# Performance work log

Measured on AMD Instinct MI355X. Metric: run time of the kernel, lower is better.

The kernel has to match this reference:

```python
import jax, jax.numpy as jnp
import numpy as np

N_NODES = 50000
NEG_SLOPE = 0.2

def _gat_conv(x, W, att_src, att_dst, bias, src, dst):
    # x: [N, in_c] -> h: [N, out_c]
    h = x @ W
    a_src = (h * att_src).sum(-1)  # [N]
    a_dst = (h * att_dst).sum(-1)  # [N]
    e = a_src[src] + a_dst[dst]    # [E]
    e = jnp.where(e > 0, e, NEG_SLOPE * e)  # LeakyReLU
    # segment softmax over destination node neighborhoods
    emax = jax.ops.segment_max(e, dst, num_segments=N_NODES)
    ee = jnp.exp(e - emax[dst])
    denom = jax.ops.segment_sum(ee, dst, num_segments=N_NODES)
    alpha = ee / denom[dst]        # [E]
    out = jax.ops.segment_sum(h[src] * alpha[:, None], dst, num_segments=N_NODES)
    return out + bias

def _with_self_loops(edge_index):
    # PyG GATConv default add_self_loops=True
    loop = jnp.arange(N_NODES, dtype=edge_index.dtype)
    src = jnp.concatenate([edge_index[0], loop])
    dst = jnp.concatenate([edge_index[1], loop])
    return src, dst

def setup_inputs() -> dict:
    key = jax.random.key(0)
    ks = jax.random.split(key, 11)
    in_c, hid_c, out_c = 256, 128, 64
    E = 800000
    x = jax.random.normal(ks[0], (N_NODES, in_c), dtype=jnp.float32)
    edge_index = jax.random.randint(ks[1], (2, E), 0, N_NODES, dtype=jnp.int64)
    s1 = 1.0 / np.sqrt(in_c)
    s2 = 1.0 / np.sqrt(hid_c)
    return {
        "x": x,
        "edge_index": edge_index,
        "W1": jax.random.normal(ks[2], (in_c, hid_c), dtype=jnp.float32) * s1,
        "att_src1": jax.random.normal(ks[3], (hid_c,), dtype=jnp.float32) * s2,
        "att_dst1": jax.random.normal(ks[4], (hid_c,), dtype=jnp.float32) * s2,
        "b1": jax.random.normal(ks[5], (hid_c,), dtype=jnp.float32) * 0.01,
        "W2": jax.random.normal(ks[6], (hid_c, out_c), dtype=jnp.float32) * s2,
        "att_src2": jax.random.normal(ks[7], (out_c,), dtype=jnp.float32) * (1.0 / np.sqrt(out_c)),
        "att_dst2": jax.random.normal(ks[8], (out_c,), dtype=jnp.float32) * (1.0 / np.sqrt(out_c)),
        "b2": jax.random.normal(ks[9], (out_c,), dtype=jnp.float32) * 0.01,
    }

def reference(x, edge_index, W1, att_src1, att_dst1, b1, W2, att_src2, att_dst2, b2):
    src, dst = _with_self_loops(edge_index)
    hid = _gat_conv(x, W1, att_src1, att_dst1, b1, src, dst)
    hid = jax.nn.relu(hid)
    out = _gat_conv(hid, W2, att_src2, att_dst2, b2, src, dst)
    return jax.nn.log_softmax(out, axis=1)
```

## Files before the change

### kernel.cpp

```cpp
#include <hip/hip_runtime.h>
#include <hip/hip_bf16.h>
#include <math.h>

#define N_NODES 50000
#define E_RAW   800000
#define E_TOT   850000
#define NEG_SLOPE 0.2f
#define CAP 64

#define NBKT   392
#define BCAP   2944
#define SCHUNK 4096
#define SB     208

typedef __attribute__((ext_vector_type(8))) short short8;
typedef __attribute__((ext_vector_type(4))) float f32x4;
typedef __attribute__((ext_vector_type(4))) unsigned short ushort4_t;

__device__ __forceinline__ short f2bf(float f) {
    __hip_bfloat16 h = __float2bfloat16(f);
    return *reinterpret_cast<short*>(&h);
}
__device__ __forceinline__ unsigned int f2bfu(float f) {
    __hip_bfloat16 h = __float2bfloat16(f);
    return (unsigned int)*reinterpret_cast<unsigned short*>(&h);
}
__device__ __forceinline__ float bflo(unsigned int u) {
    return __uint_as_float(u << 16);
}
__device__ __forceinline__ float bfhi(unsigned int u) {
    return __uint_as_float(u & 0xffff0000u);
}
__device__ __forceinline__ void fma8(float al, const uint4& h, float* acc) {
    acc[0] = fmaf(al, bflo(h.x), acc[0]);
    acc[1] = fmaf(al, bfhi(h.x), acc[1]);
    acc[2] = fmaf(al, bflo(h.y), acc[2]);
    acc[3] = fmaf(al, bfhi(h.y), acc[3]);
    acc[4] = fmaf(al, bflo(h.z), acc[4]);
    acc[5] = fmaf(al, bfhi(h.z), acc[5]);
    acc[6] = fmaf(al, bflo(h.w), acc[6]);
    acc[7] = fmaf(al, bfhi(h.w), acc[7]);
}
__device__ __forceinline__ void fma4(float al, const uint2& h, float* acc) {
    acc[0] = fmaf(al, bflo(h.x), acc[0]);
    acc[1] = fmaf(al, bfhi(h.x), acc[1]);
    acc[2] = fmaf(al, bflo(h.y), acc[2]);
    acc[3] = fmaf(al, bfhi(h.y), acc[3]);
}

template<int K, int N>
__device__ __forceinline__ void wf_body(
        int idx, const float* __restrict__ W, short* __restrict__ Wf) {
    constexpr int NT = N / 16;
    const int j  = idx & 7;
    const int n  = (idx >> 3) & 15;
    const int q  = (idx >> 7) & 3;
    const int t  = (idx >> 9) % NT;
    const int kc = idx / (512 * NT);
    const int k   = kc * 32 + q * 8 + j;
    const int col = t * 16 + n;
    Wf[idx] = f2bf(W[(size_t)k * N + col]);
}

__global__ __launch_bounds__(256) void gat_wf12_kernel(
        const float* __restrict__ W1, short* __restrict__ Wf1,
        const float* __restrict__ W2, short* __restrict__ Wf2,
        int* __restrict__ gcnt) {
    if (blockIdx.x == 0) {
        gcnt[threadIdx.x] = 0;
        gcnt[threadIdx.x + 256] = 0;
    }
    int idx = blockIdx.x * 256 + threadIdx.x;
    if (idx < 256 * 128) {
        wf_body<256, 128>(idx, W1, Wf1);
    } else {
        idx -= 256 * 128;
        if (idx < 128 * 64) wf_body<128, 64>(idx, W2, Wf2);
    }
}

template<int K, int N>
__device__ __forceinline__ void gemm_att_body(
        const int blk,
        const float* __restrict__ xf, const short* __restrict__ Wf,
        const float* __restrict__ att_src, const float* __restrict__ att_dst,
        short* __restrict__ h_bf,
        float* __restrict__ a_src, float* __restrict__ a_dst) {
    constexpr int NT = N / 16;
    constexpr int KC = K / 32;
    constexpr int PF = KC < 4 ? KC : 4;
    const int tid  = threadIdx.x;
    const int lane = tid & 63;
    const int wv   = tid >> 6;
    const int mrow = lane & 15;
    const int q    = lane >> 4;

    const int row0 = blk * 64 + wv * 16;
    const int rowA = row0 + mrow;
    const int rowAc = rowA < N_NODES ? rowA : 0;
    const float* xrow = &xf[(size_t)rowAc * K + q * 8];

    f32x4 acc[NT];
    #pragma unroll
    for (int t = 0; t < NT; ++t) acc[t] = f32x4{0.f, 0.f, 0.f, 0.f};

    float4 xa[PF], xb[PF];
    #pragma unroll
    for (int kc = 0; kc < PF; ++kc) {
        xa[kc] = *(const float4*)&xrow[kc * 32];
        xb[kc] = *(const float4*)&xrow[kc * 32 + 4];
    }

    #pragma unroll
    for (int kc = 0; kc < KC; ++kc) {
        const int sl = kc % PF;
        short8 a;
        a[0] = f2bf(xa[sl].x); a[1] = f2bf(xa[sl].y);
        a[2] = f2bf(xa[sl].z); a[3] = f2bf(xa[sl].w);
        a[4] = f2bf(xb[sl].x); a[5] = f2bf(xb[sl].y);
        a[6] = f2bf(xb[sl].z); a[7] = f2bf(xb[sl].w);
        if (kc + PF < KC) {
            xa[sl] = *(const float4*)&xrow[(kc + PF) * 32];
            xb[sl] = *(const float4*)&xrow[(kc + PF) * 32 + 4];
        }
        #pragma unroll
        for (int t = 0; t < NT; ++t) {
            const short8 b = *(const short8*)&Wf[((size_t)(kc * NT + t) * 64 + lane) * 8];
            acc[t] = __builtin_amdgcn_mfma_f32_16x16x32_bf16(a, b, acc[t], 0, 0, 0);
        }
    }

    #pragma unroll
    for (int r = 0; r < 4; ++r) {
        const int rowD = row0 + q * 4 + r;
        float ps = 0.0f, pd = 0.0f;
        #pragma unroll
        for (int t = 0; t < NT; ++t) {
            const int col = t * 16 + mrow;
            ps = fmaf(acc[t][r], att_src[col], ps);
            pd = fmaf(acc[t][r], att_dst[col], pd);
        }
        #pragma unroll
        for (int off = 8; off > 0; off >>= 1) {
            ps += __shfl_xor(ps, off);
            pd += __shfl_xor(pd, off);
        }
        if (rowD < N_NODES) {
            if (mrow == 0) { a_src[rowD] = ps; a_dst[rowD] = pd; }
            #pragma unroll
            for (int t = 0; t < NT; ++t)
                h_bf[(size_t)rowD * N + t * 16 + mrow] = f2bf(acc[t][r]);
        }
    }
}

template<int K, int N>
__global__ __launch_bounds__(256) void gat_fat1_kernel(
        const float* __restrict__ xf, const short* __restrict__ Wf,
        const float* __restrict__ att_src, const float* __restrict__ att_dst,
        short* __restrict__ h_bf,
        float* __restrict__ a_src, float* __restrict__ a_dst,
        const int* __restrict__ ei, int* __restrict__ gcnt,
        unsigned int* __restrict__ buf, int GB) {
    __shared__ int hist[NBKT];
    __shared__ int base[NBKT];
    if ((int)blockIdx.x < GB) {
        gemm_att_body<K, N>(blockIdx.x, xf, Wf,
                            att_src, att_dst, h_bf, a_src, a_dst);
    } else {
        const int sb = (int)blockIdx.x - GB;
        const int c0 = sb * SCHUNK;
        const int c1 = (c0 + SCHUNK < E_TOT) ? c0 + SCHUNK : E_TOT;
        for (int t = threadIdx.x; t < NBKT; t += 256) hist[t] = 0;
        __syncthreads();
        for (int i = c0 + threadIdx.x; i < c1; i += 256) {
            const int d = (i < E_RAW) ? ei[E_RAW + i] : (i - E_RAW);
            atomicAdd(&hist[d >> 7], 1);
        }
        __syncthreads();
        for (int t = threadIdx.x; t < NBKT; t += 256)
            base[t] = atomicAdd(&gcnt[t], hist[t]);
        __syncthreads();
        for (int t = threadIdx.x; t < NBKT; t += 256) hist[t] = 0;
        __syncthreads();
        for (int i = c0 + threadIdx.x; i < c1; i += 256) {
            int s, d;
            if (i < E_RAW) { s = ei[i]; d = ei[E_RAW + i]; }
            else           { s = d = i - E_RAW; }
            const int b = d >> 7;
            const int p = base[b] + atomicAdd(&hist[b], 1);
            if (p < BCAP)
                buf[(size_t)b * BCAP + p] =
                    ((unsigned int)s << 7) | (unsigned int)(d & 127);
        }
    }
}

__global__ __launch_bounds__(256) void gat_ell_kernel(
        const unsigned int* __restrict__ buf, const int* __restrict__ gcnt,
        int* __restrict__ cnt, unsigned short* __restrict__ srcs) {
    const int b = blockIdx.x;
    __shared__ unsigned int c2[128];
    if (threadIdx.x < 128) c2[threadIdx.x] = 0;
    __syncthreads();
    int n = gcnt[b];
    n = n < BCAP ? n : BCAP;
    const unsigned int* bb = buf + (size_t)b * BCAP;
    for (int i = threadIdx.x; i < n; i += 256) {
        const unsigned int e = bb[i];
        const int dl = (int)(e & 127u);
        const unsigned int s = e >> 7;
        const unsigned int c = atomicAdd(&c2[dl], 1u);
        if (c < CAP)
            srcs[((size_t)((b << 7) + dl) << 6) + c] = (unsigned short)s;
    }
    __syncthreads();
    const int d = (b << 7) + threadIdx.x;
    if (threadIdx.x < 128 && d < N_NODES) {
        unsigned int c = c2[threadIdx.x];
        cnt[d] = (int)(c < CAP ? c : CAP);
    }
}

__device__ __forceinline__ void softmax_stage(
        const int* __restrict__ cnt, const unsigned short* __restrict__ srcs,
        const float* __restrict__ a_src, const float* __restrict__ a_dst,
        const int d0, float* lalpha, unsigned short* lsrc,
        int* ldeg, float* ladst) {
    const int tid = threadIdx.x;
    if (tid < 16) {
        const int d = d0 + tid;
        int dg = cnt[d];
        ldeg[tid]  = dg < CAP ? dg : CAP;
        ladst[tid] = a_dst[d];
    }
    __syncthreads();
    const int dl = tid >> 4;
    const int so = (tid & 15) * 4;
    const int dg = ldeg[dl];
    const float ad = ladst[dl];
    const ushort4_t s4 =
        *(const ushort4_t*)(srcs + ((size_t)(d0 + dl) << 6) + so);
    float e[4];
    #pragma unroll
    for (int i = 0; i < 4; ++i) {
        if (so + i < dg) {
            const float t = a_src[(int)s4[i]] + ad;
            e[i] = t > 0.0f ? t : NEG_SLOPE * t;
        } else {
            e[i] = -1e30f;
        }
    }
    float m = fmaxf(fmaxf(e[0], e[1]), fmaxf(e[2], e[3]));
    #pragma unroll
    for (int off = 1; off < 16; off <<= 1) m = fmaxf(m, __shfl_xor(m, off));
    float ex[4], ss = 0.0f;
    #pragma unroll
    for (int i = 0; i < 4; ++i) { ex[i] = __expf(e[i] - m); ss += ex[i]; }
    #pragma unroll
    for (int off = 1; off < 16; off <<= 1) ss += __shfl_xor(ss, off);
    const float rinv = 1.0f / ss;
    float4 av;
    av.x = ex[0] * rinv; av.y = ex[1] * rinv;
    av.z = ex[2] * rinv; av.w = ex[3] * rinv;
    *(float4*)&lalpha[(dl << 6) + so] = av;
    *(ushort4_t*)&lsrc[(dl << 6) + so] = s4;
}

__global__ __launch_bounds__(256, 8) void gat_aggr1_fused_kernel(
        const int* __restrict__ cnt, const unsigned short* __restrict__ srcs,
        const float* __restrict__ a_src, const float* __restrict__ a_dst,
        const unsigned short* __restrict__ h_bf, const float* __restrict__ bias,
        const short* __restrict__ Wf2,
        const float* __restrict__ att_src2, const float* __restrict__ att_dst2,
        short* __restrict__ hbf2,
        float* __restrict__ a_src2, float* __restrict__ a_dst2) {
    constexpr int N = 128;
    __shared__ __align__(16) float lalpha[1024];
    __shared__ __align__(16) unsigned short lsrc[1024];
    __shared__ int   ldeg[16];
    __shared__ float ladst[16];
    __shared__ __align__(16) short lh[16 * 136];
    __shared__ float pspart[64], pdpart[64];
    const int tid = threadIdx.x;
    const int d0 = blockIdx.x * 16;

    softmax_stage(cnt, srcs, a_src, a_dst, d0, lalpha, lsrc, ldeg, ladst);
    __syncthreads();

    const int lane = tid & 63;
    const int g    = lane >> 4;
    const int sub  = lane & 15;
    const int dl   = (tid >> 6) * 4 + g;
    const int deg  = ldeg[dl];
    const int base = dl << 6;

    float acc[8];
    #pragma unroll
    for (int c = 0; c < 8; ++c) acc[c] = 0.0f;

    int j = 0;
    for (; j + 4 <= deg; j += 4) {
        const ushort4_t s4 = *(const ushort4_t*)&lsrc[base + j];
        const float4    a4 = *(const float4*)&lalpha[base + j];
        const uint4 h0 = *(const uint4*)(h_bf + (size_t)s4[0] * N + sub * 8);
        const uint4 h1 = *(const uint4*)(h_bf + (size_t)s4[1] * N + sub * 8);
        const uint4 h2 = *(const uint4*)(h_bf + (size_t)s4[2] * N + sub * 8);
        const uint4 h3 = *(const uint4*)(h_bf + (size_t)s4[3] * N + sub * 8);
        fma8(a4.x, h0, acc); fma8(a4.y, h1, acc);
        fma8(a4.z, h2, acc); fma8(a4.w, h3, acc);
    }
    if (j < deg) {
        const ushort4_t s4 = *(const ushort4_t*)&lsrc[base + j];
        const float4    a4 = *(const float4*)&lalpha[base + j];
        const int rem = deg - j;
        const uint4 h0 = *(const uint4*)(h_bf + (size_t)s4[0] * N + sub * 8);
        uint4 h1 = {0, 0, 0, 0}, h2 = {0, 0, 0, 0};
        if (rem >= 2) h1 = *(const uint4*)(h_bf + (size_t)s4[1] * N + sub * 8);
        if (rem >= 3) h2 = *(const uint4*)(h_bf + (size_t)s4[2] * N + sub * 8);
        fma8(a4.x, h0, acc); fma8(a4.y, h1, acc); fma8(a4.z, h2, acc);
    }

    {
        const float4 b0 = *(const float4*)&bias[sub * 8];
        const float4 b1 = *(const float4*)&bias[sub * 8 + 4];
        float v[8];
        v[0] = fmaxf(acc[0] + b0.x, 0.0f); v[1] = fmaxf(acc[1] + b0.y, 0.0f);
        v[2] = fmaxf(acc[2] + b0.z, 0.0f); v[3] = fmaxf(acc[3] + b0.w, 0.0f);
        v[4] = fmaxf(acc[4] + b1.x, 0.0f); v[5] = fmaxf(acc[5] + b1.y, 0.0f);
        v[6] = fmaxf(acc[6] + b1.z, 0.0f); v[7] = fmaxf(acc[7] + b1.w, 0.0f);
        uint4 p;
        p.x = f2bfu(v[0]) | (f2bfu(v[1]) << 16);
        p.y = f2bfu(v[2]) | (f2bfu(v[3]) << 16);
        p.z = f2bfu(v[4]) | (f2bfu(v[5]) << 16);
        p.w = f2bfu(v[6]) | (f2bfu(v[7]) << 16);
        *(uint4*)&lh[dl * 136 + sub * 8] = p;
    }
    __syncthreads();

    const int w    = tid >> 6;
    const int q    = lane >> 4;
    const int mrow = lane & 15;
    f32x4 acc2 = f32x4{0.f, 0.f, 0.f, 0.f};
    #pragma unroll
    for (int kc = 0; kc < 4; ++kc) {
        const short8 a = *(const short8*)&lh[mrow * 136 + q * 8 + kc * 32];
        const short8 b = *(const short8*)&Wf2[((size_t)(kc * 4 + w) * 64 + lane) * 8];
        acc2 = __builtin_amdgcn_mfma_f32_16x16x32_bf16(a, b, acc2, 0, 0, 0);
    }

    const float as2 = att_src2[w * 16 + mrow];
    const float ad2 = att_dst2[w * 16 + mrow];
    #pragma unroll
    for (int r = 0; r < 4; ++r) {
        const int rl = q * 4 + r;
        float ps = acc2[r] * as2;
        float pd = acc2[r] * ad2;
        #pragma unroll
        for (int off = 1; off < 16; off <<= 1) {
            ps += __shfl_xor(ps, off);
            pd += __shfl_xor(pd, off);
        }
        if (mrow == 0) { pspart[w * 16 + rl] = ps; pdpart[w * 16 + rl] = pd; }
        hbf2[(size_t)(d0 + rl) * 64 + w * 16 + mrow] = f2bf(acc2[r]);
    }
    __syncthreads();
    if (tid < 16) {
        a_src2[d0 + tid] = pspart[tid] + pspart[16 + tid]
                         + pspart[32 + tid] + pspart[48 + tid];
        a_dst2[d0 + tid] = pdpart[tid] + pdpart[16 + tid]
                         + pdpart[32 + tid] + pdpart[48 + tid];
    }
}

__global__ __launch_bounds__(256, 8) void gat_aggr2_kernel(
        const int* __restrict__ cnt, const unsigned short* __restrict__ srcs,
        const float* __restrict__ a_src, const float* __restrict__ a_dst,
        const unsigned short* __restrict__ h_bf, const float* __restrict__ bias,
        float* __restrict__ outf) {
    constexpr int N = 64;
    __shared__ __align__(16) float lalpha[1024];
    __shared__ __align__(16) unsigned short lsrc[1024];
    __shared__ int   ldeg[16];
    __shared__ float ladst[16];
    const int tid = threadIdx.x;
    const int d0 = blockIdx.x * 16;

    softmax_stage(cnt, srcs, a_src, a_dst, d0, lalpha, lsrc, ldeg, ladst);
    __syncthreads();

    const int lane = tid & 63;
    const int g    = lane >> 4;
    const int sub  = lane & 15;
    const int dl   = (tid >> 6) * 4 + g;
    const int d    = d0 + dl;
    const int deg  = ldeg[dl];
    const int base = dl << 6;

    float acc[4];
    #pragma unroll
    for (int c = 0; c < 4; ++c) acc[c] = 0.0f;

    int j = 0;
    for (; j + 4 <= deg; j += 4) {
        const ushort4_t s4 = *(const ushort4_t*)&lsrc[base + j];
        const float4    a4 = *(const float4*)&lalpha[base + j];
        const uint2 h0 = *(const uint2*)(h_bf + (size_t)s4[0] * N + sub * 4);
        const uint2 h1 = *(const uint2*)(h_bf + (size_t)s4[1] * N + sub * 4);
        const uint2 h2 = *(const uint2*)(h_bf + (size_t)s4[2] * N + sub * 4);
        const uint2 h3 = *(const uint2*)(h_bf + (size_t)s4[3] * N + sub * 4);
        fma4(a4.x, h0, acc); fma4(a4.y, h1, acc);
        fma4(a4.z, h2, acc); fma4(a4.w, h3, acc);
    }
    if (j < deg) {
        const ushort4_t s4 = *(const ushort4_t*)&lsrc[base + j];
        const float4    a4 = *(const float4*)&lalpha[base + j];
        const int rem = deg - j;
        const uint2 h0 = *(const uint2*)(h_bf + (size_t)s4[0] * N + sub * 4);
        uint2 h1 = {0, 0}, h2 = {0, 0};
        if (rem >= 2) h1 = *(const uint2*)(h_bf + (size_t)s4[1] * N + sub * 4);
        if (rem >= 3) h2 = *(const uint2*)(h_bf + (size_t)s4[2] * N + sub * 4);
        fma4(a4.x, h0, acc); fma4(a4.y, h1, acc); fma4(a4.z, h2, acc);
    }

    float v[4];
    #pragma unroll
    for (int c = 0; c < 4; ++c) v[c] = acc[c] + bias[sub * 4 + c];
    float mm = fmaxf(fmaxf(v[0], v[1]), fmaxf(v[2], v[3]));
    #pragma unroll
    for (int off = 1; off < 16; off <<= 1) mm = fmaxf(mm, __shfl_xor(mm, off));
    float es = __expf(v[0] - mm) + __expf(v[1] - mm)
             + __expf(v[2] - mm) + __expf(v[3] - mm);
    #pragma unroll
    for (int off = 1; off < 16; off <<= 1) es += __shfl_xor(es, off);
    const float ls = logf(es);
    float4 o;
    o.x = v[0] - mm - ls; o.y = v[1] - mm - ls;
    o.z = v[2] - mm - ls; o.w = v[3] - mm - ls;
    *(float4*)&outf[(size_t)d * N + sub * 4] = o;
}

extern "C" void kernel_launch(void* const* d_in, const int* in_sizes, int n_in,
                              void* d_out, int out_size, void* d_ws, size_t ws_size,
                              hipStream_t stream) {
    const float* x        = (const float*)d_in[0];
    const int*   ei       = (const int*)  d_in[1];
    const float* W1       = (const float*)d_in[2];
    const float* att_src1 = (const float*)d_in[3];
    const float* att_dst1 = (const float*)d_in[4];
    const float* b1       = (const float*)d_in[5];
    const float* W2       = (const float*)d_in[6];
    const float* att_src2 = (const float*)d_in[7];
    const float* att_dst2 = (const float*)d_in[8];
    const float* b2       = (const float*)d_in[9];
    float* out = (float*)d_out;
    float* ws  = (float*)d_ws;

    float* a_src1 = ws;
    float* a_dst1 = a_src1 + 50000;
    float* a_src2 = a_dst1 + 50000;
    float* a_dst2 = a_src2 + 50000;
    int*   cnt    = (int*)(a_dst2 + 50000);
    int*   gcnt   = cnt + 50000;
    unsigned int*   buf  = (unsigned int*)(gcnt + 512);
    unsigned short* srcs = (unsigned short*)(buf + (size_t)NBKT * BCAP);
    short* hbf1   = (short*)(srcs + (size_t)N_NODES * CAP);
    short* hbf2   = hbf1  + 6400000;
    short* Wf1    = hbf2  + 3200000;
    short* Wf2    = Wf1   + 32768;

    const int GB = (N_NODES + 63) / 64;

    gat_wf12_kernel<<<160, 256, 0, stream>>>(W1, Wf1, W2, Wf2, gcnt);

    gat_fat1_kernel<256, 128><<<GB + SB, 256, 0, stream>>>(
        x, Wf1, att_src1, att_dst1, hbf1, a_src1, a_dst1,
        ei, gcnt, buf, GB);

    gat_ell_kernel<<<NBKT, 256, 0, stream>>>(buf, gcnt, cnt, srcs);

    gat_aggr1_fused_kernel<<<3125, 256, 0, stream>>>(
        cnt, srcs, a_src1, a_dst1, (const unsigned short*)hbf1, b1,
        Wf2, att_src2, att_dst2, hbf2, a_src2, a_dst2);

    gat_aggr2_kernel<<<3125, 256, 0, stream>>>(
        cnt, srcs, a_src2, a_dst2, (const unsigned short*)hbf2, b2,
        out);
}
```

Baseline: 200.7 us.

## Split layer-1 aggregation into column-sliced kernel plus separate layer-2 GEMM

The fused layer-1 aggregation plus layer-2 GEMM kernel is split in two. A column-sliced aggregation kernel launches four times as many blocks, each handling a 32-column slice and splitting edges across lanes with a shuffle reduction, and writes relu(agg+bias) to a new bf16 buffer. A separate MFMA GEMM kernel then produces h2, with a_src2/a_dst2 computed from precomputed W2·att vectors. Padded source indices (set to 0) let both aggregation loops drop their remainder branches. The split adds a 12.8MB round trip through global memory and an extra launch, and the softmax stage is recomputed once per slice.

Result: slower. 221.8 us (+10.5%).

```diff
diff --git a/kernel.cpp b/kernel.cpp
--- a/kernel.cpp
+++ b/kernel.cpp
@@ -30,6 +30,9 @@
 }
 __device__ __forceinline__ float bfhi(unsigned int u) {
     return __uint_as_float(u & 0xffff0000u);
+}
+__device__ __forceinline__ float bf2f(short v) {
+    return __uint_as_float(((unsigned int)(unsigned short)v) << 16);
 }
 __device__ __forceinline__ void fma8(float al, const uint4& h, float* acc) {
     acc[0] = fmaf(al, bflo(h.x), acc[0]);
@@ -65,10 +68,22 @@
 __global__ __launch_bounds__(256) void gat_wf12_kernel(
         const float* __restrict__ W1, short* __restrict__ Wf1,
         const float* __restrict__ W2, short* __restrict__ Wf2,
+        const float* __restrict__ att_src2, const float* __restrict__ att_dst2,
+        float* __restrict__ wtS, float* __restrict__ wtD,
         int* __restrict__ gcnt) {
     if (blockIdx.x == 0) {
         gcnt[threadIdx.x] = 0;
         gcnt[threadIdx.x + 256] = 0;
+        if (threadIdx.x < 128) {
+            float s = 0.0f, d = 0.0f;
+            for (int n = 0; n < 64; ++n) {
+                const float w = W2[threadIdx.x * 64 + n];
+                s = fmaf(w, att_src2[n], s);
+                d = fmaf(w, att_dst2[n], d);
+            }
+            wtS[threadIdx.x] = s;
+            wtD[threadIdx.x] = d;
+        }
     }
     int idx = blockIdx.x * 256 + threadIdx.x;
     if (idx < 256 * 128) {
@@ -242,13 +257,16 @@
     const ushort4_t s4 =
         *(const ushort4_t*)(srcs + ((size_t)(d0 + dl) << 6) + so);
     float e[4];
+    ushort4_t s4w;
     #pragma unroll
     for (int i = 0; i < 4; ++i) {
         if (so + i < dg) {
             const float t = a_src[(int)s4[i]] + ad;
             e[i] = t > 0.0f ? t : NEG_SLOPE * t;
+            s4w[i] = s4[i];
         } else {
             e[i] = -1e30f;
+            s4w[i] = 0;
         }
     }
     float m = fmaxf(fmaxf(e[0], e[1]), fmaxf(e[2], e[3]));
@@ -264,66 +282,67 @@
     av.x = ex[0] * rinv; av.y = ex[1] * rinv;
     av.z = ex[2] * rinv; av.w = ex[3] * rinv;
     *(float4*)&lalpha[(dl << 6) + so] = av;
-    *(ushort4_t*)&lsrc[(dl << 6) + so] = s4;
-}
-
-__global__ __launch_bounds__(256, 8) void gat_aggr1_fused_kernel(
+    *(ushort4_t*)&lsrc[(dl << 6) + so] = s4w;
+}
+
+__global__ __launch_bounds__(256, 8) void gat_aggr1s_kernel(
         const int* __restrict__ cnt, const unsigned short* __restrict__ srcs,
         const float* __restrict__ a_src, const float* __restrict__ a_dst,
         const unsigned short* __restrict__ h_bf, const float* __restrict__ bias,
-        const short* __restrict__ Wf2,
-        const float* __restrict__ att_src2, const float* __restrict__ att_dst2,
-        short* __restrict__ hbf2,
-        float* __restrict__ a_src2, float* __restrict__ a_dst2) {
-    constexpr int N = 128;
+        short* __restrict__ agg1) {
     __shared__ __align__(16) float lalpha[1024];
     __shared__ __align__(16) unsigned short lsrc[1024];
     __shared__ int   ldeg[16];
     __shared__ float ladst[16];
-    __shared__ __align__(16) short lh[16 * 136];
-    __shared__ float pspart[64], pdpart[64];
-    const int tid = threadIdx.x;
-    const int d0 = blockIdx.x * 16;
+    const int tid   = threadIdx.x;
+    const int slice = blockIdx.x & 3;
+    const int d0    = (blockIdx.x >> 2) * 16;
 
     softmax_stage(cnt, srcs, a_src, a_dst, d0, lalpha, lsrc, ldeg, ladst);
     __syncthreads();
 
     const int lane = tid & 63;
-    const int g    = lane >> 4;
-    const int sub  = lane & 15;
-    const int dl   = (tid >> 6) * 4 + g;
+    const int wv   = tid >> 6;
+    const int gq   = lane >> 4;
+    const int e    = (lane >> 2) & 3;
+    const int c4   = lane & 3;
+    const int dl   = wv * 4 + gq;
     const int deg  = ldeg[dl];
     const int base = dl << 6;
+    const int col0 = slice * 32 + c4 * 8;
 
     float acc[8];
     #pragma unroll
     for (int c = 0; c < 8; ++c) acc[c] = 0.0f;
 
+    const int deg4 = (deg + 3) & ~3;
     int j = 0;
-    for (; j + 4 <= deg; j += 4) {
-        const ushort4_t s4 = *(const ushort4_t*)&lsrc[base + j];
-        const float4    a4 = *(const float4*)&lalpha[base + j];
-        const uint4 h0 = *(const uint4*)(h_bf + (size_t)s4[0] * N + sub * 8);
-        const uint4 h1 = *(const uint4*)(h_bf + (size_t)s4[1] * N + sub * 8);
-        const uint4 h2 = *(const uint4*)(h_bf + (size_t)s4[2] * N + sub * 8);
-        const uint4 h3 = *(const uint4*)(h_bf + (size_t)s4[3] * N + sub * 8);
-        fma8(a4.x, h0, acc); fma8(a4.y, h1, acc);
-        fma8(a4.z, h2, acc); fma8(a4.w, h3, acc);
-    }
-    if (j < deg) {
-        const ushort4_t s4 = *(const ushort4_t*)&lsrc[base + j];
-        const float4    a4 = *(const float4*)&lalpha[base + j];
-        const int rem = deg - j;
-        const uint4 h0 = *(const uint4*)(h_bf + (size_t)s4[0] * N + sub * 8);
-        uint4 h1 = {0, 0, 0, 0}, h2 = {0, 0, 0, 0};
-        if (rem >= 2) h1 = *(const uint4*)(h_bf + (size_t)s4[1] * N + sub * 8);
-        if (rem >= 3) h2 = *(const uint4*)(h_bf + (size_t)s4[2] * N + sub * 8);
-        fma8(a4.x, h0, acc); fma8(a4.y, h1, acc); fma8(a4.z, h2, acc);
-    }
-
-    {
-        const float4 b0 = *(const float4*)&bias[sub * 8];
-        const float4 b1 = *(const float4*)&bias[sub * 8 + 4];
+    for (; j + 8 <= deg4; j += 8) {
+        const int s0    = (int)lsrc[base + j + e];
+        const int s1    = (int)lsrc[base + j + 4 + e];
+        const float al0 = lalpha[base + j + e];
+        const float al1 = lalpha[base + j + 4 + e];
+        const uint4 h0 = *(const uint4*)(h_bf + (size_t)s0 * 128 + col0);
+        const uint4 h1 = *(const uint4*)(h_bf + (size_t)s1 * 128 + col0);
+        fma8(al0, h0, acc);
+        fma8(al1, h1, acc);
+    }
+    if (j < deg4) {
+        const int s0    = (int)lsrc[base + j + e];
+        const float al0 = lalpha[base + j + e];
+        const uint4 h0 = *(const uint4*)(h_bf + (size_t)s0 * 128 + col0);
+        fma8(al0, h0, acc);
+    }
+
+    #pragma unroll
+    for (int c = 0; c < 8; ++c) {
+        acc[c] += __shfl_xor(acc[c], 4);
+        acc[c] += __shfl_xor(acc[c], 8);
+    }
+
+    if (e == 0) {
+        const float4 b0 = *(const float4*)&bias[col0];
+        const float4 b1 = *(const float4*)&bias[col0 + 4];
         float v[8];
         v[0] = fmaxf(acc[0] + b0.x, 0.0f); v[1] = fmaxf(acc[1] + b0.y, 0.0f);
         v[2] = fmaxf(acc[2] + b0.z, 0.0f); v[3] = fmaxf(acc[3] + b0.w, 0.0f);
@@ -334,42 +353,60 @@
         p.y = f2bfu(v[2]) | (f2bfu(v[3]) << 16);
         p.z = f2bfu(v[4]) | (f2bfu(v[5]) << 16);
         p.w = f2bfu(v[6]) | (f2bfu(v[7]) << 16);
-        *(uint4*)&lh[dl * 136 + sub * 8] = p;
-    }
-    __syncthreads();
-
-    const int w    = tid >> 6;
+        *(uint4*)&agg1[(size_t)(d0 + dl) * 128 + col0] = p;
+    }
+}
+
+__global__ __launch_bounds__(256) void gat_gemm2_kernel(
+        const short* __restrict__ agg1, const short* __restrict__ Wf2,
+        const float* __restrict__ wtS, const float* __restrict__ wtD,
+        short* __restrict__ hbf2,
+        float* __restrict__ a_src2, float* __restrict__ a_dst2) {
+    const int tid  = threadIdx.x;
+    const int lane = tid & 63;
+    const int wv   = tid >> 6;
+    const int mrow = lane & 15;
     const int q    = lane >> 4;
-    const int mrow = lane & 15;
-    f32x4 acc2 = f32x4{0.f, 0.f, 0.f, 0.f};
+    const int row0 = blockIdx.x * 64 + wv * 16;
+    const int rowA = row0 + mrow;
+    const int rowAc = rowA < N_NODES ? rowA : 0;
+
+    f32x4 acc[4];
+    #pragma unroll
+    for (int t = 0; t < 4; ++t) acc[t] = f32x4{0.f, 0.f, 0.f, 0.f};
+    float ps = 0.0f, pd = 0.0f;
+
     #pragma unroll
     for (int kc = 0; kc < 4; ++kc) {
-        const short8 a = *(const short8*)&lh[mrow * 136 + q * 8 + kc * 32];
-        const short8 b = *(const short8*)&Wf2[((size_t)(kc * 4 + w) * 64 + lane) * 8];
-        acc2 = __builtin_amdgcn_mfma_f32_16x16x32_bf16(a, b, acc2, 0, 0, 0);
-    }
-
-    const float as2 = att_src2[w * 16 + mrow];
-    const float ad2 = att_dst2[w * 16 + mrow];
+        const short8 a = *(const short8*)&agg1[(size_t)rowAc * 128 + kc * 32 + q * 8];
+        #pragma unroll
+        for (int jj = 0; jj < 8; ++jj) {
+            const float av = bf2f(a[jj]);
+            ps = fmaf(av, wtS[kc * 32 + q * 8 + jj], ps);
+            pd = fmaf(av, wtD[kc * 32 + q * 8 + jj], pd);
+        }
+        #pragma unroll
+        for (int t = 0; t < 4; ++t) {
+            const short8 b = *(const short8*)&Wf2[((size_t)(kc * 4 + t) * 64 + lane) * 8];
+            acc[t] = __builtin_amdgcn_mfma_f32_16x16x32_bf16(a, b, acc[t], 0, 0, 0);
+        }
+    }
+
+    ps += __shfl_xor(ps, 16); ps += __shfl_xor(ps, 32);
+    pd += __shfl_xor(pd, 16); pd += __shfl_xor(pd, 32);
+    if (lane < 16 && rowA < N_NODES) {
+        a_src2[rowA] = ps;
+        a_dst2[rowA] = pd;
+    }
+
     #pragma unroll
     for (int r = 0; r < 4; ++r) {
-        const int rl = q * 4 + r;
-        float ps = acc2[r] * as2;
-        float pd = acc2[r] * ad2;
-        #pragma unroll
-        for (int off = 1; off < 16; off <<= 1) {
-            ps += __shfl_xor(ps, off);
-            pd += __shfl_xor(pd, off);
-        }
-        if (mrow == 0) { pspart[w * 16 + rl] = ps; pdpart[w * 16 + rl] = pd; }
-        hbf2[(size_t)(d0 + rl) * 64 + w * 16 + mrow] = f2bf(acc2[r]);
-    }
-    __syncthreads();
-    if (tid < 16) {
-        a_src2[d0 + tid] = pspart[tid] + pspart[16 + tid]
-                         + pspart[32 + tid] + pspart[48 + tid];
-        a_dst2[d0 + tid] = pdpart[tid] + pdpart[16 + tid]
-                         + pdpart[32 + tid] + pdpart[48 + tid];
+        const int rowD = row0 + q * 4 + r;
+        if (rowD < N_NODES) {
+            #pragma unroll
+            for (int t = 0; t < 4; ++t)
+                hbf2[(size_t)rowD * 64 + t * 16 + mrow] = f2bf(acc[t][r]);
+        }
     }
 }
 
@@ -401,8 +438,8 @@
     #pragma unroll
     for (int c = 0; c < 4; ++c) acc[c] = 0.0f;
 
-    int j = 0;
-    for (; j + 4 <= deg; j += 4) {
+    const int deg4 = (deg + 3) & ~3;
+    for (int j = 0; j < deg4; j += 4) {
         const ushort4_t s4 = *(const ushort4_t*)&lsrc[base + j];
         const float4    a4 = *(const float4*)&lalpha[base + j];
         const uint2 h0 = *(const uint2*)(h_bf + (size_t)s4[0] * N + sub * 4);
@@ -411,16 +448,6 @@
         const uint2 h3 = *(const uint2*)(h_bf + (size_t)s4[3] * N + sub * 4);
         fma4(a4.x, h0, acc); fma4(a4.y, h1, acc);
         fma4(a4.z, h2, acc); fma4(a4.w, h3, acc);
-    }
-    if (j < deg) {
-        const ushort4_t s4 = *(const ushort4_t*)&lsrc[base + j];
-        const float4    a4 = *(const float4*)&lalpha[base + j];
-        const int rem = deg - j;
-        const uint2 h0 = *(const uint2*)(h_bf + (size_t)s4[0] * N + sub * 4);
-        uint2 h1 = {0, 0}, h2 = {0, 0};
-        if (rem >= 2) h1 = *(const uint2*)(h_bf + (size_t)s4[1] * N + sub * 4);
-        if (rem >= 3) h2 = *(const uint2*)(h_bf + (size_t)s4[2] * N + sub * 4);
-        fma4(a4.x, h0, acc); fma4(a4.y, h1, acc); fma4(a4.z, h2, acc);
     }
 
     float v[4];
@@ -462,16 +489,20 @@
     float* a_dst2 = a_src2 + 50000;
     int*   cnt    = (int*)(a_dst2 + 50000);
     int*   gcnt   = cnt + 50000;
-    unsigned int*   buf  = (unsigned int*)(gcnt + 512);
+    float* wtS    = (float*)(gcnt + 512);
+    float* wtD    = wtS + 128;
+    unsigned int*   buf  = (unsigned int*)(wtD + 128);
     unsigned short* srcs = (unsigned short*)(buf + (size_t)NBKT * BCAP);
     short* hbf1   = (short*)(srcs + (size_t)N_NODES * CAP);
-    short* hbf2   = hbf1  + 6400000;
+    short* agg1   = hbf1  + 6400000;
+    short* hbf2   = agg1  + 6400000;
     short* Wf1    = hbf2  + 3200000;
     short* Wf2    = Wf1   + 32768;
 
     const int GB = (N_NODES + 63) / 64;
 
-    gat_wf12_kernel<<<160, 256, 0, stream>>>(W1, Wf1, W2, Wf2, gcnt);
+    gat_wf12_kernel<<<160, 256, 0, stream>>>(
+        W1, Wf1, W2, Wf2, att_src2, att_dst2, wtS, wtD, gcnt);
 
     gat_fat1_kernel<256, 128><<<GB + SB, 256, 0, stream>>>(
         x, Wf1, att_src1, att_dst1, hbf1, a_src1, a_dst1,
@@ -479,9 +510,11 @@
 
     gat_ell_kernel<<<NBKT, 256, 0, stream>>>(buf, gcnt, cnt, srcs);
 
-    gat_aggr1_fused_kernel<<<3125, 256, 0, stream>>>(
-        cnt, srcs, a_src1, a_dst1, (const unsigned short*)hbf1, b1,
-        Wf2, att_src2, att_dst2, hbf2, a_src2, a_dst2);
+    gat_aggr1s_kernel<<<3125 * 4, 256, 0, stream>>>(
+        cnt, srcs, a_src1, a_dst1, (const unsigned short*)hbf1, b1, agg1);
+
+    gat_gemm2_kernel<<<GB, 256, 0, stream>>>(
+        agg1, Wf2, wtS, wtD, hbf2, a_src2, a_dst2);
 
     gat_aggr2_kernel<<<3125, 256, 0, stream>>>(
         cnt, srcs, a_src2, a_dst2, (const unsigned short*)hbf2, b2,
```
